# Performance work log

Hardware: AMD Instinct MI355X
Metric: run time of the kernel (lower is better)

## Reference

```python
import jax, jax.numpy as jnp
import numpy as np

NQ = 14            # n_qubits
NB = 2             # n_blocks
KLOC = 4           # k_local
K = 2 ** KLOC      # Hermitian observable dim = 16
NOFF = K * (K - 1) // 2   # 120 off-diagonal params
DEPTH = 3          # vqc_depth
IN_DIM = 784
OUT_DIM = 10
BATCH = 128
GROUPS = [list(range(s, s + KLOC)) for s in range(NQ - KLOC + 1)]  # sliding k-local groups
NOBS = len(GROUPS)  # 11
TOTAL_ENC = NB * ((NQ // 2) + ((NQ - 1) // 2)) * 15  # 390 SU(4) encoding params

# 15 two-qubit Pauli words in PennyLane's lexicographic IXYZ order (identity excluded)
_I = np.eye(2, dtype=np.complex64)
_X = np.array([[0, 1], [1, 0]], np.complex64)
_Y = np.array([[0, -1j], [1j, 0]], np.complex64)
_Z = np.array([[1, 0], [0, -1]], np.complex64)
_P = {'I': _I, 'X': _X, 'Y': _Y, 'Z': _Z}
_WORDS = [a + b for a in 'IXYZ' for b in 'IXYZ'][1:]
P15 = jnp.asarray(np.stack([np.kron(_P[w[0]], _P[w[1]]) for w in _WORDS]))  # (15,4,4)
CNOT = jnp.asarray(np.array([[1, 0, 0, 0], [0, 1, 0, 0], [0, 0, 0, 1], [0, 0, 1, 0]], np.complex64))
_ROWS, _COLS = np.tril_indices(K, -1)  # row-major lower-tri order == create_Hermitian fill order


def su4(theta):
    """PennyLane SpecialUnitary: U = expm(i * sum_m theta_m P_m), theta: (B,15).
    The generator is Hermitian, so use eigh instead of generic expm."""
    Hm = jnp.einsum('bm,mij->bij', theta.astype(jnp.complex64), P15)  # (B,4,4) Hermitian
    w, V = jnp.linalg.eigh(Hm)
    return jnp.einsum('bij,bj,bkj->bik', V, jnp.exp(1j * w.astype(jnp.complex64)), V.conj())


def apply_gate(state, U, wires):
    """Apply a k-qubit gate U ((B,2^k,2^k) or (2^k,2^k)) to state (B, 2,...,2)."""
    n = state.ndim - 1
    k = len(wires)
    axes = [w + 1 for w in wires]
    perm = [0] + axes + [a for a in range(1, n + 1) if a not in axes]
    st = jnp.transpose(state, perm)
    shp = st.shape
    st = st.reshape(shp[0], 2 ** k, -1)
    if U.ndim == 3:
        st = jnp.einsum('bij,bjr->bir', U, st)
    else:
        st = jnp.einsum('ij,bjr->bir', U, st)
    return jnp.transpose(st.reshape(shp), np.argsort(perm))


def expval_herm(state, H, wires):
    """<psi| H_{wires} |psi> per batch element."""
    n = state.ndim - 1
    axes = [w + 1 for w in wires]
    perm = [0] + axes + [a for a in range(1, n + 1) if a not in axes]
    st = jnp.transpose(state, perm).reshape(state.shape[0], H.shape[0], -1)
    return jnp.einsum('bkr,kl,blr->b', st.conj(), H, st).real


def create_hermitian(A, Bp, D):
    """Faithful port of create_Hermitian: lower-tri A+iB (row-major), diag D[1:] on
    positions 0..K-2 (D[0] unused, last diag 0), then H = h + h^dagger (diag doubled)."""
    h = jnp.zeros((K, K), jnp.complex64).at[_ROWS, _COLS].set(A + 1j * Bp)
    d = jnp.zeros((K,), A.dtype).at[jnp.arange(K - 1)].set(D[1:])
    h = h + jnp.diag(d).astype(jnp.complex64)
    return h + h.conj().T


def ry_mat(theta):
    c = jnp.cos(theta / 2)
    s = jnp.sin(theta / 2)
    return jnp.stack([jnp.stack([c, -s]), jnp.stack([s, c])]).astype(jnp.complex64)


def setup_inputs():
    key = jax.random.key(0)
    ks = jax.random.split(key, 9)
    lim = 1.0 / np.sqrt(IN_DIM)
    lim_h = 1.0 / np.sqrt(NOBS)
    return {
        'x': jax.random.normal(ks[0], (BATCH, IN_DIM), jnp.float32),
        'W_enc': jax.random.uniform(ks[1], (TOTAL_ENC, IN_DIM), jnp.float32, -lim, lim),
        'b_enc': jax.random.uniform(ks[2], (TOTAL_ENC,), jnp.float32, -lim, lim),
        'var_params': 0.01 * jax.random.normal(ks[3], (DEPTH, NQ), jnp.float32),
        'A': 2.0 * jax.random.normal(ks[4], (NOBS, NOFF), jnp.float32),
        'Bp': 2.0 * jax.random.normal(ks[5], (NOBS, NOFF), jnp.float32),
        'D': 2.0 * jax.random.normal(ks[6], (NOBS, K), jnp.float32),
        'W_head': jax.random.uniform(ks[7], (OUT_DIM, NOBS), jnp.float32, -lim_h, lim_h),
        'b_head': jax.random.uniform(ks[8], (OUT_DIM,), jnp.float32, -lim_h, lim_h),
    }


def reference(x, W_enc, b_enc, var_params, A, Bp, D, W_head, b_head):
    encoded = x @ W_enc.T + b_enc                      # (B, 390)
    Hs = jax.vmap(create_hermitian)(A, Bp, D)          # (NOBS, K, K)
    Bsz = x.shape[0]
    state = jnp.zeros((Bsz,) + (2,) * NQ, jnp.complex64).at[(slice(None),) + (0,) * NQ].set(1.0)
    # SU(4) brick-layer encoding: even pairs then odd pairs per block
    idx = 0
    for _ in range(NB):
        for q in list(range(0, NQ - 1, 2)) + list(range(1, NQ - 1, 2)):
            state = apply_gate(state, su4(encoded[:, idx:idx + 15]), [q, q + 1])
            idx += 15
    # variational RY + CNOT brick layers
    for layer in range(DEPTH):
        for q in range(NQ):
            state = apply_gate(state, ry_mat(var_params[layer, q]), [q])
        for q in list(range(0, NQ - 1, 2)) + list(range(1, NQ - 1, 2)):
            state = apply_gate(state, CNOT, [q, q + 1])
    q_out = jnp.stack([expval_herm(state, Hs[w], GROUPS[w]) for w in range(NOBS)], axis=1)
    q_out = q_out.astype(jnp.float32)                  # (B, NOBS)
    return q_out @ W_head.T + b_head                   # (B, OUT_DIM)
```

## Files before the change

kernel.cpp:

```cpp
#include <hip/hip_runtime.h>
#include <math.h>

#define NQ      14
#define NSTATE  16384
#define BATCH   128
#define DEPTH   3
#define NOBS    11
#define KDIM    16
#define NOFF    120
#define INDIM   784
#define OUTDIM  10

__device__ __forceinline__ int F2(int a) { return a + (a >> 4); }
#define PHYS2 (NSTATE + (NSTATE >> 4))

__device__ __forceinline__ float sbc(float x) {
  return __int_as_float(__builtin_amdgcn_readfirstlane(__float_as_int(x)));
}

__global__ __launch_bounds__(256) void enc_expm_kernel(
    const float* __restrict__ x, const float* __restrict__ W,
    const float* __restrict__ bvec, float2* __restrict__ Ubuf)
{
  int wave = ((blockIdx.x << 2) | (threadIdx.x >> 6));
  int lane = threadIdx.x & 63;
  int g = wave >> 7;
  int b = wave & 127;

  const float4* x4 = (const float4*)(x + (size_t)b * INDIM);
  const float4* w4 = (const float4*)(W + (size_t)g * 15 * INDIM);

  float acc[15];
#pragma unroll
  for (int m = 0; m < 15; ++m) acc[m] = 0.f;
#pragma unroll
  for (int it = 0; it < 4; ++it) {
    int j4 = lane + it * 64;
    if (j4 < 196) {
      float4 xv = x4[j4];
#pragma unroll
      for (int m = 0; m < 15; ++m) {
        float4 wv = w4[m * 196 + j4];
        acc[m] = fmaf(xv.x, wv.x, fmaf(xv.y, wv.y, fmaf(xv.z, wv.z, fmaf(xv.w, wv.w, acc[m]))));
      }
    }
  }
#pragma unroll
  for (int m = 0; m < 15; ++m) {
#pragma unroll
    for (int off = 32; off; off >>= 1) acc[m] += __shfl_xor(acc[m], off);
  }

  if (lane < 4) {
    const int j = lane;
    float th[15];
#pragma unroll
    for (int m = 0; m < 15; ++m) th[m] = acc[m] + bvec[g * 15 + m];

    const float pr_[4][4] = {{1,0,0,1},{0,1,1,0},{0,0,0,0},{1,0,0,-1}};
    const float pi_[4][4] = {{0,0,0,0},{0,0,0,0},{0,-1,1,0},{0,0,0,0}};
    float Hre[16], Him[16];
#pragma unroll
    for (int e = 0; e < 16; ++e) { Hre[e] = 0.f; Him[e] = 0.f; }
    float tsum = 0.f;
#pragma unroll
    for (int m = 0; m < 15; ++m) {
      float tv = th[m];
      tsum += fabsf(tv);
      const int code = m + 1;
      const int a = code >> 2, c = code & 3;
#pragma unroll
      for (int i = 0; i < 4; ++i)
#pragma unroll
        for (int jj = 0; jj < 4; ++jj) {
          float ar = pr_[a][(i >> 1) * 2 + (jj >> 1)], ai = pi_[a][(i >> 1) * 2 + (jj >> 1)];
          float br = pr_[c][(i & 1) * 2 + (jj & 1)],   bi = pi_[c][(i & 1) * 2 + (jj & 1)];
          Hre[i * 4 + jj] += tv * (ar * br - ai * bi);
          Him[i * 4 + jj] += tv * (ar * bi + ai * br);
        }
    }
    int s = 0;
    if (tsum > 0.25f) {
      s = (int)ceilf(log2f(tsum * 4.0f));
      if (s < 0) s = 0;
      if (s > 14) s = 14;
    }
    float sc = exp2f((float)(-s));
    float Gre[16], Gim[16];
#pragma unroll
    for (int e = 0; e < 16; ++e) { Gre[e] = -Him[e] * sc; Gim[e] = Hre[e] * sc; }

    float Tcr[4], Tci[4];
#pragma unroll
    for (int i = 0; i < 4; ++i) {
      Tcr[i] = Gre[i * 4 + j] * (1.f / 9.f) + ((i == j) ? 1.f : 0.f);
      Tci[i] = Gim[i * 4 + j] * (1.f / 9.f);
    }
#pragma unroll
    for (int k = 8; k >= 1; --k) {
      float nr[4], ni[4];
      float invk = 1.0f / (float)k;
#pragma unroll
      for (int i = 0; i < 4; ++i) {
        float xr = 0.f, xi = 0.f;
#pragma unroll
        for (int l = 0; l < 4; ++l) {
          xr = fmaf(Gre[i * 4 + l], Tcr[l], fmaf(-Gim[i * 4 + l], Tci[l], xr));
          xi = fmaf(Gre[i * 4 + l], Tci[l], fmaf( Gim[i * 4 + l], Tcr[l], xi));
        }
        nr[i] = invk * xr + ((i == j) ? 1.f : 0.f);
        ni[i] = invk * xi;
      }
#pragma unroll
      for (int i = 0; i < 4; ++i) { Tcr[i] = nr[i]; Tci[i] = ni[i]; }
    }
    for (int it = 0; it < s; ++it) {
      float nr[4] = {0.f, 0.f, 0.f, 0.f}, ni[4] = {0.f, 0.f, 0.f, 0.f};
#pragma unroll
      for (int l = 0; l < 4; ++l) {
        float tlr = Tcr[l], tli = Tci[l];
#pragma unroll
        for (int i = 0; i < 4; ++i) {
          float br = __shfl(Tcr[i], l);
          float bi = __shfl(Tci[i], l);
          nr[i] = fmaf(br, tlr, fmaf(-bi, tli, nr[i]));
          ni[i] = fmaf(br, tli, fmaf( bi, tlr, ni[i]));
        }
      }
#pragma unroll
      for (int i = 0; i < 4; ++i) { Tcr[i] = nr[i]; Tci[i] = ni[i]; }
    }
#pragma unroll
    for (int i = 0; i < 4; ++i)
      Ubuf[(size_t)wave * 16 + i * 4 + j] = make_float2(Tcr[i], Tci[i]);
  }
}

template<int S>
__device__ __forceinline__ int grpbase(int t) {
  return ((t >> S) << (S + 4)) | (t & ((1 << S) - 1));
}
template<int S>
__device__ __forceinline__ void ldgrp(const float2* st, int base, float* vr, float* vi) {
#pragma unroll
  for (int k = 0; k < 16; ++k) {
    float2 v = st[F2(base + (k << S))];
    vr[k] = v.x; vi[k] = v.y;
  }
}
template<int S>
__device__ __forceinline__ void stgrp(float2* st, int base, const float* vr, const float* vi) {
#pragma unroll
  for (int k = 0; k < 16; ++k) st[F2(base + (k << S))] = make_float2(vr[k], vi[k]);
}
__device__ __forceinline__ int base2s(int t) {
  return ((t >> 7) << 11) | (((t >> 5) & 3) << 7) | (t & 31);
}
__device__ __forceinline__ int addr2s(int base, int k) {
  return base + ((k >> 2) << 9) + ((k & 3) << 5);
}
__device__ __forceinline__ void ldgrp2(const float2* st, int base, float* vr, float* vi) {
#pragma unroll
  for (int k = 0; k < 16; ++k) {
    float2 v = st[F2(addr2s(base, k))];
    vr[k] = v.x; vi[k] = v.y;
  }
}
__device__ __forceinline__ void stgrp2(float2* st, int base, const float* vr, const float* vi) {
#pragma unroll
  for (int k = 0; k < 16; ++k) st[F2(addr2s(base, k))] = make_float2(vr[k], vi[k]);
}

__device__ __forceinline__ void loadU(const float2* __restrict__ Ug, float* ur, float* ui) {
#pragma unroll
  for (int e = 0; e < 16; ++e) {
    float2 u = Ug[e];
    ur[e] = sbc(u.x); ui[e] = sbc(u.y);
  }
}

__device__ __forceinline__ void applyU_hi(float* vr, float* vi, const float* ur, const float* ui) {
#pragma unroll
  for (int j2 = 0; j2 < 4; ++j2) {
    float ar[4], ai[4];
#pragma unroll
    for (int j = 0; j < 4; ++j) { ar[j] = vr[4 * j + j2]; ai[j] = vi[4 * j + j2]; }
#pragma unroll
    for (int i = 0; i < 4; ++i) {
      float xr = 0.f, xi = 0.f;
#pragma unroll
      for (int j = 0; j < 4; ++j) {
        xr = fmaf(ur[4 * i + j], ar[j], fmaf(-ui[4 * i + j], ai[j], xr));
        xi = fmaf(ur[4 * i + j], ai[j], fmaf( ui[4 * i + j], ar[j], xi));
      }
      vr[4 * i + j2] = xr; vi[4 * i + j2] = xi;
    }
  }
}
__device__ __forceinline__ void applyU_lo(float* vr, float* vi, const float* ur, const float* ui) {
#pragma unroll
  for (int i2 = 0; i2 < 4; ++i2) {
    float ar[4], ai[4];
#pragma unroll
    for (int j = 0; j < 4; ++j) { ar[j] = vr[4 * i2 + j]; ai[j] = vi[4 * i2 + j]; }
#pragma unroll
    for (int i = 0; i < 4; ++i) {
      float xr = 0.f, xi = 0.f;
#pragma unroll
      for (int j = 0; j < 4; ++j) {
        xr = fmaf(ur[4 * i + j], ar[j], fmaf(-ui[4 * i + j], ai[j], xr));
        xi = fmaf(ur[4 * i + j], ai[j], fmaf( ui[4 * i + j], ar[j], xi));
      }
      vr[4 * i2 + i] = xr; vi[4 * i2 + i] = xi;
    }
  }
}
__device__ __forceinline__ void applyU_mid(float* vr, float* vi, const float* ur, const float* ui) {
#pragma unroll
  for (int o = 0; o < 4; ++o) {
    const int kb = ((o >> 1) << 3) | (o & 1);
    float ar[4], ai[4];
#pragma unroll
    for (int j = 0; j < 4; ++j) { ar[j] = vr[kb | (j << 1)]; ai[j] = vi[kb | (j << 1)]; }
#pragma unroll
    for (int i = 0; i < 4; ++i) {
      float xr = 0.f, xi = 0.f;
#pragma unroll
      for (int j = 0; j < 4; ++j) {
        xr = fmaf(ur[4 * i + j], ar[j], fmaf(-ui[4 * i + j], ai[j], xr));
        xi = fmaf(ur[4 * i + j], ai[j], fmaf( ui[4 * i + j], ar[j], xi));
      }
      vr[kb | (i << 1)] = xr; vi[kb | (i << 1)] = xi;
    }
  }
}

template<int B>
__device__ __forceinline__ void ry16(float* vr, float* vi, float c, float s) {
#pragma unroll
  for (int k = 0; k < 16; ++k) {
    if (!(k & (1 << B))) {
      const int k1 = k | (1 << B);
      float r0 = vr[k], i0 = vi[k], r1 = vr[k1], i1 = vi[k1];
      vr[k]  = fmaf(c, r0, -s * r1);  vi[k]  = fmaf(c, i0, -s * i1);
      vr[k1] = fmaf(s, r0,  c * r1);  vi[k1] = fmaf(s, i0,  c * i1);
    }
  }
}
template<int CB, int TB>
__device__ __forceinline__ void cx16(float* vr, float* vi) {
#pragma unroll
  for (int k = 0; k < 16; ++k) {
    if ((k & (1 << CB)) && !(k & (1 << TB))) {
      const int k1 = k | (1 << TB);
      float tr = vr[k]; vr[k] = vr[k1]; vr[k1] = tr;
      float ti = vi[k]; vi[k] = vi[k1]; vi[k1] = ti;
    }
  }
}

template<int S>
__device__ __forceinline__ void enc_pass3(float2* st, const float2* __restrict__ U,
                                          int gHi, int gLo, int gMid, int b, int t) {
  float ur[16], ui[16], vr[16], vi[16];
  int base = grpbase<S>(t);
  ldgrp<S>(st, base, vr, vi);
  loadU(U + ((size_t)gHi  * BATCH + b) * 16, ur, ui); applyU_hi (vr, vi, ur, ui);
  loadU(U + ((size_t)gLo  * BATCH + b) * 16, ur, ui); applyU_lo (vr, vi, ur, ui);
  loadU(U + ((size_t)gMid * BATCH + b) * 16, ur, ui); applyU_mid(vr, vi, ur, ui);
  stgrp<S>(st, base, vr, vi);
}
__device__ __forceinline__ void enc_passD(float2* st, const float2* __restrict__ U,
                                          int gLo, int gMid, int b, int t) {
  float ur[16], ui[16], vr[16], vi[16];
  int base = t << 4;
  ldgrp<0>(st, base, vr, vi);
  loadU(U + ((size_t)gLo  * BATCH + b) * 16, ur, ui); applyU_lo (vr, vi, ur, ui);
  loadU(U + ((size_t)gMid * BATCH + b) * 16, ur, ui); applyU_mid(vr, vi, ur, ui);
  stgrp<0>(st, base, vr, vi);
}
__device__ __forceinline__ void enc_passE(float2* st, const float2* __restrict__ U,
                                          int gA, int gB, int b, int t) {
  float ur[16], ui[16], vr[16], vi[16];
  int base = base2s(t);
  ldgrp2(st, base, vr, vi);
  loadU(U + ((size_t)gA * BATCH + b) * 16, ur, ui); applyU_hi(vr, vi, ur, ui);
  loadU(U + ((size_t)gB * BATCH + b) * 16, ur, ui); applyU_lo(vr, vi, ur, ui);
  stgrp2(st, base, vr, vi);
}
template<int S>
__device__ __forceinline__ void var_pass3(float2* st, const float* __restrict__ vp,
                                          int l, int qbase, int t) {
  float vr[16], vi[16];
  int base = grpbase<S>(t);
  ldgrp<S>(st, base, vr, vi);
  float c[4], sn[4];
#pragma unroll
  for (int i = 0; i < 4; ++i) {
    float a = sbc(vp[l * NQ + qbase + i]) * 0.5f;
    c[i] = cosf(a); sn[i] = sinf(a);
  }
  ry16<3>(vr, vi, c[0], sn[0]);
  ry16<2>(vr, vi, c[1], sn[1]);
  ry16<1>(vr, vi, c[2], sn[2]);
  ry16<0>(vr, vi, c[3], sn[3]);
  cx16<3, 2>(vr, vi);
  cx16<1, 0>(vr, vi);
  cx16<2, 1>(vr, vi);
  stgrp<S>(st, base, vr, vi);
}
__device__ __forceinline__ void var_passD(float2* st, const float* __restrict__ vp,
                                          int l, int t) {
  float vr[16], vi[16];
  int base = t << 4;
  ldgrp<0>(st, base, vr, vi);
  float a0 = sbc(vp[l * NQ + 12]) * 0.5f;
  float a1 = sbc(vp[l * NQ + 13]) * 0.5f;
  ry16<1>(vr, vi, cosf(a0), sinf(a0));
  ry16<0>(vr, vi, cosf(a1), sinf(a1));
  cx16<1, 0>(vr, vi);
  cx16<2, 1>(vr, vi);
  stgrp<0>(st, base, vr, vi);
}
__device__ __forceinline__ void var_passE(float2* st, int t) {
  float vr[16], vi[16];
  int base = base2s(t);
  ldgrp2(st, base, vr, vi);
  cx16<3, 2>(vr, vi);
  cx16<1, 0>(vr, vi);
  stgrp2(st, base, vr, vi);
}

__global__ __launch_bounds__(1024) void qsim_kernel(
    const float2* __restrict__ U, const float* __restrict__ var_params,
    const float* __restrict__ A, const float* __restrict__ Bp,
    const float* __restrict__ D, const float* __restrict__ Wh,
    const float* __restrict__ bh, float* __restrict__ out)
{
  __shared__ float2 st[PHYS2];
  __shared__ float red[6][16];

  const int t = threadIdx.x;
  const int b = blockIdx.x >> 1;
  const int h = blockIdx.x & 1;
  const int nw = h ? 5 : 6;

  for (int i = t; i < PHYS2; i += 1024)
    st[i] = (i == 0) ? make_float2(1.f, 0.f) : make_float2(0.f, 0.f);
  __syncthreads();

  for (int nb = 0; nb < 2; ++nb) {
    int gI = nb * 13;
    enc_pass3<10>(st, U, gI + 0, gI + 1, gI + 7,  b, t); __syncthreads();
    enc_pass3<6 >(st, U, gI + 2, gI + 3, gI + 9,  b, t); __syncthreads();
    enc_pass3<2 >(st, U, gI + 4, gI + 5, gI + 11, b, t); __syncthreads();
    enc_passD    (st, U, gI + 6, gI + 12,         b, t); __syncthreads();
    enc_passE    (st, U, gI + 8, gI + 10,         b, t); __syncthreads();
  }

  for (int l = 0; l < DEPTH; ++l) {
    var_pass3<10>(st, var_params, l, 0, t); __syncthreads();
    var_pass3<6 >(st, var_params, l, 4, t); __syncthreads();
    var_pass3<2 >(st, var_params, l, 8, t); __syncthreads();
    var_passD    (st, var_params, l,    t); __syncthreads();
    var_passE    (st, t);                   __syncthreads();
  }

  const int wave = t >> 6;
  for (int idx = 0; idx < nw; ++idx) {
    const int w = 2 * idx + h;
    const float* __restrict__ Aw = A + w * NOFF;
    const float* __restrict__ Bw = Bp + w * NOFF;
    const float* __restrict__ Dw = D + w * KDIM;
    const int shift = 10 - w;
    const int hi2 = t >> shift;
    const int lo = t & ((1 << shift) - 1);
    const int base2 = (hi2 << (shift + 4)) | lo;
    float sr[16], si[16];
#pragma unroll
    for (int k = 0; k < 16; ++k) {
      float2 v = st[F2(base2 + (k << shift))];
      sr[k] = v.x; si[k] = v.y;
    }
    float yr[16], yi[16];
#pragma unroll
    for (int k = 0; k < 16; ++k) {
      float dk = (k < 15) ? Dw[k + 1] : 0.f;
      yr[k] = dk * sr[k];
      yi[k] = dk * si[k];
    }
#pragma unroll
    for (int k = 1; k < 16; ++k) {
#pragma unroll
      for (int l2 = 0; l2 < k; ++l2) {
        const int pidx = (k * (k - 1)) / 2 + l2;
        const float a = Aw[pidx];
        const float q = Bw[pidx];
        yr[k] = fmaf(a, sr[l2], fmaf(-q, si[l2], yr[k]));
        yi[k] = fmaf(a, si[l2], fmaf( q, sr[l2], yi[k]));
      }
    }
    float E = 0.f;
#pragma unroll
    for (int k = 0; k < 16; ++k)
      E = fmaf(sr[k], yr[k], fmaf(si[k], yi[k], E));
    E *= 2.0f;
#pragma unroll
    for (int off = 32; off; off >>= 1) E += __shfl_xor(E, off);
    if ((t & 63) == 0) red[idx][wave] = E;
  }
  __syncthreads();

  if (t < OUTDIM) {
    float o = (h == 0) ? bh[t] : 0.f;
    for (int idx = 0; idx < nw; ++idx) {
      const int w = 2 * idx + h;
      float q = 0.f;
#pragma unroll
      for (int ww = 0; ww < 16; ++ww) q += red[idx][ww];
      o = fmaf(Wh[t * NOBS + w], q, o);
    }
    atomicAdd(&out[b * OUTDIM + t], o);
  }
}

extern "C" void kernel_launch(void* const* d_in, const int* in_sizes, int n_in,
                              void* d_out, int out_size, void* d_ws, size_t ws_size,
                              hipStream_t stream) {
  const float* x          = (const float*)d_in[0];
  const float* W_enc      = (const float*)d_in[1];
  const float* b_enc      = (const float*)d_in[2];
  const float* var_params = (const float*)d_in[3];
  const float* A          = (const float*)d_in[4];
  const float* Bp         = (const float*)d_in[5];
  const float* D          = (const float*)d_in[6];
  const float* W_head     = (const float*)d_in[7];
  const float* b_head     = (const float*)d_in[8];
  float* out = (float*)d_out;

  float2* Ubuf = (float2*)d_ws;

  hipMemsetAsync(out, 0, (size_t)out_size * sizeof(float), stream);
  enc_expm_kernel<<<832, 256, 0, stream>>>(x, W_enc, b_enc, Ubuf);
  qsim_kernel<<<256, 1024, 0, stream>>>(Ubuf, var_params, A, Bp, D,
                                        W_head, b_head, out);
}
```

Baseline: 188.0 us.

## Split encoding GEMV and SU(4) expm into separate kernels with dense lanes

```diff
diff --git a/kernel.cpp b/kernel.cpp
--- a/kernel.cpp
+++ b/kernel.cpp
@@ -18,9 +18,9 @@
   return __int_as_float(__builtin_amdgcn_readfirstlane(__float_as_int(x)));
 }
 
-__global__ __launch_bounds__(256) void enc_expm_kernel(
+__global__ __launch_bounds__(256) void enc_kernel(
     const float* __restrict__ x, const float* __restrict__ W,
-    const float* __restrict__ bvec, float2* __restrict__ Ubuf)
+    const float* __restrict__ bvec, float* __restrict__ theta)
 {
   int wave = ((blockIdx.x << 2) | (threadIdx.x >> 6));
   int lane = threadIdx.x & 63;
@@ -50,90 +50,101 @@
 #pragma unroll
     for (int off = 32; off; off >>= 1) acc[m] += __shfl_xor(acc[m], off);
   }
-
-  if (lane < 4) {
-    const int j = lane;
-    float th[15];
-#pragma unroll
-    for (int m = 0; m < 15; ++m) th[m] = acc[m] + bvec[g * 15 + m];
-
-    const float pr_[4][4] = {{1,0,0,1},{0,1,1,0},{0,0,0,0},{1,0,0,-1}};
-    const float pi_[4][4] = {{0,0,0,0},{0,0,0,0},{0,-1,1,0},{0,0,0,0}};
-    float Hre[16], Him[16];
-#pragma unroll
-    for (int e = 0; e < 16; ++e) { Hre[e] = 0.f; Him[e] = 0.f; }
-    float tsum = 0.f;
-#pragma unroll
-    for (int m = 0; m < 15; ++m) {
-      float tv = th[m];
-      tsum += fabsf(tv);
-      const int code = m + 1;
-      const int a = code >> 2, c = code & 3;
-#pragma unroll
-      for (int i = 0; i < 4; ++i)
-#pragma unroll
-        for (int jj = 0; jj < 4; ++jj) {
-          float ar = pr_[a][(i >> 1) * 2 + (jj >> 1)], ai = pi_[a][(i >> 1) * 2 + (jj >> 1)];
-          float br = pr_[c][(i & 1) * 2 + (jj & 1)],   bi = pi_[c][(i & 1) * 2 + (jj & 1)];
-          Hre[i * 4 + jj] += tv * (ar * br - ai * bi);
-          Him[i * 4 + jj] += tv * (ar * bi + ai * br);
-        }
-    }
-    int s = 0;
-    if (tsum > 0.25f) {
-      s = (int)ceilf(log2f(tsum * 4.0f));
-      if (s < 0) s = 0;
-      if (s > 14) s = 14;
-    }
-    float sc = exp2f((float)(-s));
-    float Gre[16], Gim[16];
-#pragma unroll
-    for (int e = 0; e < 16; ++e) { Gre[e] = -Him[e] * sc; Gim[e] = Hre[e] * sc; }
-
-    float Tcr[4], Tci[4];
+  if (lane == 0) {
+#pragma unroll
+    for (int m = 0; m < 15; ++m) theta[(size_t)wave * 15 + m] = acc[m] + bvec[g * 15 + m];
+  }
+}
+
+__global__ __launch_bounds__(256) void expm_kernel(
+    const float* __restrict__ theta, float2* __restrict__ Ubuf)
+{
+  int gid  = blockIdx.x * 256 + threadIdx.x;
+  int pair = gid >> 2;
+  int j    = gid & 3;
+  int lane = threadIdx.x & 63;
+  int grp  = lane & 60;
+
+  const float* th = theta + (size_t)pair * 15;
+
+  const float pr_[4][4] = {{1,0,0,1},{0,1,1,0},{0,0,0,0},{1,0,0,-1}};
+  const float pi_[4][4] = {{0,0,0,0},{0,0,0,0},{0,-1,1,0},{0,0,0,0}};
+
+  float Hre[16], Him[16];
+#pragma unroll
+  for (int e = 0; e < 16; ++e) { Hre[e] = 0.f; Him[e] = 0.f; }
+  float tsum = 0.f;
+#pragma unroll
+  for (int m = 0; m < 15; ++m) {
+    float tv = th[m];
+    tsum += fabsf(tv);
+    const int code = m + 1;
+    const int a = code >> 2, c = code & 3;
+#pragma unroll
+    for (int i = 0; i < 4; ++i)
+#pragma unroll
+      for (int jj = 0; jj < 4; ++jj) {
+        float ar = pr_[a][(i >> 1) * 2 + (jj >> 1)], ai = pi_[a][(i >> 1) * 2 + (jj >> 1)];
+        float br = pr_[c][(i & 1) * 2 + (jj & 1)],   bi = pi_[c][(i & 1) * 2 + (jj & 1)];
+        Hre[i * 4 + jj] += tv * (ar * br - ai * bi);
+        Him[i * 4 + jj] += tv * (ar * bi + ai * br);
+      }
+  }
+  int s = 0;
+  if (tsum > 0.25f) {
+    s = (int)ceilf(log2f(tsum * 4.0f));
+    if (s < 0) s = 0;
+    if (s > 14) s = 14;
+  }
+  float sc = exp2f((float)(-s));
+  float Gre[16], Gim[16];
+#pragma unroll
+  for (int e = 0; e < 16; ++e) { Gre[e] = -Him[e] * sc; Gim[e] = Hre[e] * sc; }
+
+  float Tcr[4], Tci[4];
+#pragma unroll
+  for (int i = 0; i < 4; ++i) {
+    Tcr[i] = Gre[i * 4 + j] * (1.f / 9.f) + ((i == j) ? 1.f : 0.f);
+    Tci[i] = Gim[i * 4 + j] * (1.f / 9.f);
+  }
+#pragma unroll
+  for (int k = 8; k >= 1; --k) {
+    float nr[4], ni[4];
+    float invk = 1.0f / (float)k;
 #pragma unroll
     for (int i = 0; i < 4; ++i) {
-      Tcr[i] = Gre[i * 4 + j] * (1.f / 9.f) + ((i == j) ? 1.f : 0.f);
-      Tci[i] = Gim[i * 4 + j] * (1.f / 9.f);
-    }
-#pragma unroll
-    for (int k = 8; k >= 1; --k) {
-      float nr[4], ni[4];
-      float invk = 1.0f / (float)k;
+      float xr = 0.f, xi = 0.f;
+#pragma unroll
+      for (int l = 0; l < 4; ++l) {
+        xr = fmaf(Gre[i * 4 + l], Tcr[l], fmaf(-Gim[i * 4 + l], Tci[l], xr));
+        xi = fmaf(Gre[i * 4 + l], Tci[l], fmaf( Gim[i * 4 + l], Tcr[l], xi));
+      }
+      nr[i] = invk * xr + ((i == j) ? 1.f : 0.f);
+      ni[i] = invk * xi;
+    }
+#pragma unroll
+    for (int i = 0; i < 4; ++i) { Tcr[i] = nr[i]; Tci[i] = ni[i]; }
+  }
+  for (int it = 0; it < s; ++it) {
+    float nr[4] = {0.f, 0.f, 0.f, 0.f}, ni[4] = {0.f, 0.f, 0.f, 0.f};
+#pragma unroll
+    for (int l = 0; l < 4; ++l) {
+      int src = grp | l;
+      float tlr = Tcr[l], tli = Tci[l];
 #pragma unroll
       for (int i = 0; i < 4; ++i) {
-        float xr = 0.f, xi = 0.f;
-#pragma unroll
-        for (int l = 0; l < 4; ++l) {
-          xr = fmaf(Gre[i * 4 + l], Tcr[l], fmaf(-Gim[i * 4 + l], Tci[l], xr));
-          xi = fmaf(Gre[i * 4 + l], Tci[l], fmaf( Gim[i * 4 + l], Tcr[l], xi));
-        }
-        nr[i] = invk * xr + ((i == j) ? 1.f : 0.f);
-        ni[i] = invk * xi;
-      }
-#pragma unroll
-      for (int i = 0; i < 4; ++i) { Tcr[i] = nr[i]; Tci[i] = ni[i]; }
-    }
-    for (int it = 0; it < s; ++it) {
-      float nr[4] = {0.f, 0.f, 0.f, 0.f}, ni[4] = {0.f, 0.f, 0.f, 0.f};
-#pragma unroll
-      for (int l = 0; l < 4; ++l) {
-        float tlr = Tcr[l], tli = Tci[l];
-#pragma unroll
-        for (int i = 0; i < 4; ++i) {
-          float br = __shfl(Tcr[i], l);
-          float bi = __shfl(Tci[i], l);
-          nr[i] = fmaf(br, tlr, fmaf(-bi, tli, nr[i]));
-          ni[i] = fmaf(br, tli, fmaf( bi, tlr, ni[i]));
-        }
-      }
-#pragma unroll
-      for (int i = 0; i < 4; ++i) { Tcr[i] = nr[i]; Tci[i] = ni[i]; }
-    }
-#pragma unroll
-    for (int i = 0; i < 4; ++i)
-      Ubuf[(size_t)wave * 16 + i * 4 + j] = make_float2(Tcr[i], Tci[i]);
-  }
+        float br = __shfl(Tcr[i], src);
+        float bi = __shfl(Tci[i], src);
+        nr[i] = fmaf(br, tlr, fmaf(-bi, tli, nr[i]));
+        ni[i] = fmaf(br, tli, fmaf( bi, tlr, ni[i]));
+      }
+    }
+#pragma unroll
+    for (int i = 0; i < 4; ++i) { Tcr[i] = nr[i]; Tci[i] = ni[i]; }
+  }
+#pragma unroll
+  for (int i = 0; i < 4; ++i)
+    Ubuf[(size_t)pair * 16 + i * 4 + j] = make_float2(Tcr[i], Tci[i]);
 }
 
 template<int S>
@@ -438,10 +449,13 @@
   const float* b_head     = (const float*)d_in[8];
   float* out = (float*)d_out;
 
-  float2* Ubuf = (float2*)d_ws;
+  float*  theta = (float*)d_ws;
+  size_t  thBytes = (size_t)3328 * 15 * sizeof(float);
+  float2* Ubuf = (float2*)((char*)d_ws + ((thBytes + 255) / 256) * 256);
 
   hipMemsetAsync(out, 0, (size_t)out_size * sizeof(float), stream);
-  enc_expm_kernel<<<832, 256, 0, stream>>>(x, W_enc, b_enc, Ubuf);
+  enc_kernel <<<832, 256, 0, stream>>>(x, W_enc, b_enc, theta);
+  expm_kernel<<<52,  256, 0, stream>>>(theta, Ubuf);
   qsim_kernel<<<256, 1024, 0, stream>>>(Ubuf, var_params, A, Bp, D,
                                         W_head, b_head, out);
 }
```

Measured after the change: 176.6 us. 6.1% less time.

## Fuse SU(4) encoding expm into simulation kernel and add separate head kernel

Applied to the files above, without the earlier changes.

```diff
diff --git a/kernel.cpp b/kernel.cpp
--- a/kernel.cpp
+++ b/kernel.cpp
@@ -18,124 +18,6 @@
   return __int_as_float(__builtin_amdgcn_readfirstlane(__float_as_int(x)));
 }
 
-__global__ __launch_bounds__(256) void enc_expm_kernel(
-    const float* __restrict__ x, const float* __restrict__ W,
-    const float* __restrict__ bvec, float2* __restrict__ Ubuf)
-{
-  int wave = ((blockIdx.x << 2) | (threadIdx.x >> 6));
-  int lane = threadIdx.x & 63;
-  int g = wave >> 7;
-  int b = wave & 127;
-
-  const float4* x4 = (const float4*)(x + (size_t)b * INDIM);
-  const float4* w4 = (const float4*)(W + (size_t)g * 15 * INDIM);
-
-  float acc[15];
-#pragma unroll
-  for (int m = 0; m < 15; ++m) acc[m] = 0.f;
-#pragma unroll
-  for (int it = 0; it < 4; ++it) {
-    int j4 = lane + it * 64;
-    if (j4 < 196) {
-      float4 xv = x4[j4];
-#pragma unroll
-      for (int m = 0; m < 15; ++m) {
-        float4 wv = w4[m * 196 + j4];
-        acc[m] = fmaf(xv.x, wv.x, fmaf(xv.y, wv.y, fmaf(xv.z, wv.z, fmaf(xv.w, wv.w, acc[m]))));
-      }
-    }
-  }
-#pragma unroll
-  for (int m = 0; m < 15; ++m) {
-#pragma unroll
-    for (int off = 32; off; off >>= 1) acc[m] += __shfl_xor(acc[m], off);
-  }
-
-  if (lane < 4) {
-    const int j = lane;
-    float th[15];
-#pragma unroll
-    for (int m = 0; m < 15; ++m) th[m] = acc[m] + bvec[g * 15 + m];
-
-    const float pr_[4][4] = {{1,0,0,1},{0,1,1,0},{0,0,0,0},{1,0,0,-1}};
-    const float pi_[4][4] = {{0,0,0,0},{0,0,0,0},{0,-1,1,0},{0,0,0,0}};
-    float Hre[16], Him[16];
-#pragma unroll
-    for (int e = 0; e < 16; ++e) { Hre[e] = 0.f; Him[e] = 0.f; }
-    float tsum = 0.f;
-#pragma unroll
-    for (int m = 0; m < 15; ++m) {
-      float tv = th[m];
-      tsum += fabsf(tv);
-      const int code = m + 1;
-      const int a = code >> 2, c = code & 3;
-#pragma unroll
-      for (int i = 0; i < 4; ++i)
-#pragma unroll
-        for (int jj = 0; jj < 4; ++jj) {
-          float ar = pr_[a][(i >> 1) * 2 + (jj >> 1)], ai = pi_[a][(i >> 1) * 2 + (jj >> 1)];
-          float br = pr_[c][(i & 1) * 2 + (jj & 1)],   bi = pi_[c][(i & 1) * 2 + (jj & 1)];
-          Hre[i * 4 + jj] += tv * (ar * br - ai * bi);
-          Him[i * 4 + jj] += tv * (ar * bi + ai * br);
-        }
-    }
-    int s = 0;
-    if (tsum > 0.25f) {
-      s = (int)ceilf(log2f(tsum * 4.0f));
-      if (s < 0) s = 0;
-      if (s > 14) s = 14;
-    }
-    float sc = exp2f((float)(-s));
-    float Gre[16], Gim[16];
-#pragma unroll
-    for (int e = 0; e < 16; ++e) { Gre[e] = -Him[e] * sc; Gim[e] = Hre[e] * sc; }
-
-    float Tcr[4], Tci[4];
-#pragma unroll
-    for (int i = 0; i < 4; ++i) {
-      Tcr[i] = Gre[i * 4 + j] * (1.f / 9.f) + ((i == j) ? 1.f : 0.f);
-      Tci[i] = Gim[i * 4 + j] * (1.f / 9.f);
-    }
-#pragma unroll
-    for (int k = 8; k >= 1; --k) {
-      float nr[4], ni[4];
-      float invk = 1.0f / (float)k;
-#pragma unroll
-      for (int i = 0; i < 4; ++i) {
-        float xr = 0.f, xi = 0.f;
-#pragma unroll
-        for (int l = 0; l < 4; ++l) {
-          xr = fmaf(Gre[i * 4 + l], Tcr[l], fmaf(-Gim[i * 4 + l], Tci[l], xr));
-          xi = fmaf(Gre[i * 4 + l], Tci[l], fmaf( Gim[i * 4 + l], Tcr[l], xi));
-        }
-        nr[i] = invk * xr + ((i == j) ? 1.f : 0.f);
-        ni[i] = invk * xi;
-      }
-#pragma unroll
-      for (int i = 0; i < 4; ++i) { Tcr[i] = nr[i]; Tci[i] = ni[i]; }
-    }
-    for (int it = 0; it < s; ++it) {
-      float nr[4] = {0.f, 0.f, 0.f, 0.f}, ni[4] = {0.f, 0.f, 0.f, 0.f};
-#pragma unroll
-      for (int l = 0; l < 4; ++l) {
-        float tlr = Tcr[l], tli = Tci[l];
-#pragma unroll
-        for (int i = 0; i < 4; ++i) {
-          float br = __shfl(Tcr[i], l);
-          float bi = __shfl(Tci[i], l);
-          nr[i] = fmaf(br, tlr, fmaf(-bi, tli, nr[i]));
-          ni[i] = fmaf(br, tli, fmaf( bi, tlr, ni[i]));
-        }
-      }
-#pragma unroll
-      for (int i = 0; i < 4; ++i) { Tcr[i] = nr[i]; Tci[i] = ni[i]; }
-    }
-#pragma unroll
-    for (int i = 0; i < 4; ++i)
-      Ubuf[(size_t)wave * 16 + i * 4 + j] = make_float2(Tcr[i], Tci[i]);
-  }
-}
-
 template<int S>
 __device__ __forceinline__ int grpbase(int t) {
   return ((t >> S) << (S + 4)) | (t & ((1 << S) - 1));
@@ -171,11 +53,11 @@
   for (int k = 0; k < 16; ++k) st[F2(addr2s(base, k))] = make_float2(vr[k], vi[k]);
 }
 
-__device__ __forceinline__ void loadU(const float2* __restrict__ Ug, float* ur, float* ui) {
+__device__ __forceinline__ void loadU(const float2* Ul, float* ur, float* ui) {
 #pragma unroll
   for (int e = 0; e < 16; ++e) {
-    float2 u = Ug[e];
-    ur[e] = sbc(u.x); ui[e] = sbc(u.y);
+    float2 u = Ul[e];
+    ur[e] = u.x; ui[e] = u.y;
   }
 }
 
@@ -260,32 +142,32 @@
 }
 
 template<int S>
-__device__ __forceinline__ void enc_pass3(float2* st, const float2* __restrict__ U,
-                                          int gHi, int gLo, int gMid, int b, int t) {
+__device__ __forceinline__ void enc_pass3(float2* st, const float2* Ulds,
+                                          int gHi, int gLo, int gMid, int t) {
   float ur[16], ui[16], vr[16], vi[16];
   int base = grpbase<S>(t);
   ldgrp<S>(st, base, vr, vi);
-  loadU(U + ((size_t)gHi  * BATCH + b) * 16, ur, ui); applyU_hi (vr, vi, ur, ui);
-  loadU(U + ((size_t)gLo  * BATCH + b) * 16, ur, ui); applyU_lo (vr, vi, ur, ui);
-  loadU(U + ((size_t)gMid * BATCH + b) * 16, ur, ui); applyU_mid(vr, vi, ur, ui);
+  loadU(Ulds + gHi  * 16, ur, ui); applyU_hi (vr, vi, ur, ui);
+  loadU(Ulds + gLo  * 16, ur, ui); applyU_lo (vr, vi, ur, ui);
+  loadU(Ulds + gMid * 16, ur, ui); applyU_mid(vr, vi, ur, ui);
   stgrp<S>(st, base, vr, vi);
 }
-__device__ __forceinline__ void enc_passD(float2* st, const float2* __restrict__ U,
-                                          int gLo, int gMid, int b, int t) {
+__device__ __forceinline__ void enc_passD(float2* st, const float2* Ulds,
+                                          int gLo, int gMid, int t) {
   float ur[16], ui[16], vr[16], vi[16];
   int base = t << 4;
   ldgrp<0>(st, base, vr, vi);
-  loadU(U + ((size_t)gLo  * BATCH + b) * 16, ur, ui); applyU_lo (vr, vi, ur, ui);
-  loadU(U + ((size_t)gMid * BATCH + b) * 16, ur, ui); applyU_mid(vr, vi, ur, ui);
+  loadU(Ulds + gLo  * 16, ur, ui); applyU_lo (vr, vi, ur, ui);
+  loadU(Ulds + gMid * 16, ur, ui); applyU_mid(vr, vi, ur, ui);
   stgrp<0>(st, base, vr, vi);
 }
-__device__ __forceinline__ void enc_passE(float2* st, const float2* __restrict__ U,
-                                          int gA, int gB, int b, int t) {
+__device__ __forceinline__ void enc_passE(float2* st, const float2* Ulds,
+                                          int gA, int gB, int t) {
   float ur[16], ui[16], vr[16], vi[16];
   int base = base2s(t);
   ldgrp2(st, base, vr, vi);
-  loadU(U + ((size_t)gA * BATCH + b) * 16, ur, ui); applyU_hi(vr, vi, ur, ui);
-  loadU(U + ((size_t)gB * BATCH + b) * 16, ur, ui); applyU_lo(vr, vi, ur, ui);
+  loadU(Ulds + gA * 16, ur, ui); applyU_hi(vr, vi, ur, ui);
+  loadU(Ulds + gB * 16, ur, ui); applyU_lo(vr, vi, ur, ui);
   stgrp2(st, base, vr, vi);
 }
 template<int S>
@@ -331,31 +213,146 @@
   stgrp2(st, base, vr, vi);
 }
 
-__global__ __launch_bounds__(1024) void qsim_kernel(
-    const float2* __restrict__ U, const float* __restrict__ var_params,
+__global__ __launch_bounds__(1024) void qfm_kernel(
+    const float* __restrict__ x, const float* __restrict__ W,
+    const float* __restrict__ bvec, const float* __restrict__ var_params,
     const float* __restrict__ A, const float* __restrict__ Bp,
-    const float* __restrict__ D, const float* __restrict__ Wh,
-    const float* __restrict__ bh, float* __restrict__ out)
+    const float* __restrict__ D, float* __restrict__ qws)
 {
   __shared__ float2 st[PHYS2];
+  __shared__ float2 Ulds[26 * 16];
   __shared__ float red[6][16];
 
   const int t = threadIdx.x;
   const int b = blockIdx.x >> 1;
   const int h = blockIdx.x & 1;
   const int nw = h ? 5 : 6;
+  const int wv = t >> 6;
+  const int lane = t & 63;
 
   for (int i = t; i < PHYS2; i += 1024)
     st[i] = (i == 0) ? make_float2(1.f, 0.f) : make_float2(0.f, 0.f);
+
+  const float4* x4 = (const float4*)(x + (size_t)b * INDIM);
+  for (int r = 0; r < 2; ++r) {
+    const int g = r * 13 + wv;
+    if (wv < 13) {
+      const float4* w4 = (const float4*)(W + (size_t)g * 15 * INDIM);
+      float acc[15];
+#pragma unroll
+      for (int m = 0; m < 15; ++m) acc[m] = 0.f;
+#pragma unroll
+      for (int it = 0; it < 4; ++it) {
+        int j4 = lane + it * 64;
+        if (j4 < 196) {
+          float4 xv = x4[j4];
+#pragma unroll
+          for (int m = 0; m < 15; ++m) {
+            float4 wvv = w4[m * 196 + j4];
+            acc[m] = fmaf(xv.x, wvv.x, fmaf(xv.y, wvv.y, fmaf(xv.z, wvv.z, fmaf(xv.w, wvv.w, acc[m]))));
+          }
+        }
+      }
+#pragma unroll
+      for (int m = 0; m < 15; ++m) {
+#pragma unroll
+        for (int off = 32; off; off >>= 1) acc[m] += __shfl_xor(acc[m], off);
+      }
+
+      if (lane < 4) {
+        const int j = lane;
+        float th[15];
+#pragma unroll
+        for (int m = 0; m < 15; ++m) th[m] = acc[m] + bvec[g * 15 + m];
+
+        const float pr_[4][4] = {{1,0,0,1},{0,1,1,0},{0,0,0,0},{1,0,0,-1}};
+        const float pi_[4][4] = {{0,0,0,0},{0,0,0,0},{0,-1,1,0},{0,0,0,0}};
+        float Hre[16], Him[16];
+#pragma unroll
+        for (int e = 0; e < 16; ++e) { Hre[e] = 0.f; Him[e] = 0.f; }
+        float tsum = 0.f;
+#pragma unroll
+        for (int m = 0; m < 15; ++m) {
+          float tv = th[m];
+          tsum += fabsf(tv);
+          const int code = m + 1;
+          const int a = code >> 2, c = code & 3;
+#pragma unroll
+          for (int i = 0; i < 4; ++i)
+#pragma unroll
+            for (int jj = 0; jj < 4; ++jj) {
+              float ar = pr_[a][(i >> 1) * 2 + (jj >> 1)], ai = pi_[a][(i >> 1) * 2 + (jj >> 1)];
+              float br = pr_[c][(i & 1) * 2 + (jj & 1)],   bi = pi_[c][(i & 1) * 2 + (jj & 1)];
+              Hre[i * 4 + jj] += tv * (ar * br - ai * bi);
+              Him[i * 4 + jj] += tv * (ar * bi + ai * br);
+            }
+        }
+        int s = 0;
+        if (tsum > 0.25f) {
+          s = (int)ceilf(log2f(tsum * 4.0f));
+          if (s < 0) s = 0;
+          if (s > 14) s = 14;
+        }
+        float sc = exp2f((float)(-s));
+        float Gre[16], Gim[16];
+#pragma unroll
+        for (int e = 0; e < 16; ++e) { Gre[e] = -Him[e] * sc; Gim[e] = Hre[e] * sc; }
+
+        float Tcr[4], Tci[4];
+#pragma unroll
+        for (int i = 0; i < 4; ++i) {
+          Tcr[i] = Gre[i * 4 + j] * (1.f / 9.f) + ((i == j) ? 1.f : 0.f);
+          Tci[i] = Gim[i * 4 + j] * (1.f / 9.f);
+        }
+#pragma unroll
+        for (int k = 8; k >= 1; --k) {
+          float nr[4], ni[4];
+          float invk = 1.0f / (float)k;
+#pragma unroll
+          for (int i = 0; i < 4; ++i) {
+            float xr = 0.f, xi = 0.f;
+#pragma unroll
+            for (int l = 0; l < 4; ++l) {
+              xr = fmaf(Gre[i * 4 + l], Tcr[l], fmaf(-Gim[i * 4 + l], Tci[l], xr));
+              xi = fmaf(Gre[i * 4 + l], Tci[l], fmaf( Gim[i * 4 + l], Tcr[l], xi));
+            }
+            nr[i] = invk * xr + ((i == j) ? 1.f : 0.f);
+            ni[i] = invk * xi;
+          }
+#pragma unroll
+          for (int i = 0; i < 4; ++i) { Tcr[i] = nr[i]; Tci[i] = ni[i]; }
+        }
+        for (int it = 0; it < s; ++it) {
+          float nr[4] = {0.f, 0.f, 0.f, 0.f}, ni[4] = {0.f, 0.f, 0.f, 0.f};
+#pragma unroll
+          for (int l = 0; l < 4; ++l) {
+            float tlr = Tcr[l], tli = Tci[l];
+#pragma unroll
+            for (int i = 0; i < 4; ++i) {
+              float br = __shfl(Tcr[i], l);
+              float bi = __shfl(Tci[i], l);
+              nr[i] = fmaf(br, tlr, fmaf(-bi, tli, nr[i]));
+              ni[i] = fmaf(br, tli, fmaf( bi, tlr, ni[i]));
+            }
+          }
+#pragma unroll
+          for (int i = 0; i < 4; ++i) { Tcr[i] = nr[i]; Tci[i] = ni[i]; }
+        }
+#pragma unroll
+        for (int i = 0; i < 4; ++i)
+          Ulds[g * 16 + i * 4 + j] = make_float2(Tcr[i], Tci[i]);
+      }
+    }
+  }
   __syncthreads();
 
   for (int nb = 0; nb < 2; ++nb) {
     int gI = nb * 13;
-    enc_pass3<10>(st, U, gI + 0, gI + 1, gI + 7,  b, t); __syncthreads();
-    enc_pass3<6 >(st, U, gI + 2, gI + 3, gI + 9,  b, t); __syncthreads();
-    enc_pass3<2 >(st, U, gI + 4, gI + 5, gI + 11, b, t); __syncthreads();
-    enc_passD    (st, U, gI + 6, gI + 12,         b, t); __syncthreads();
-    enc_passE    (st, U, gI + 8, gI + 10,         b, t); __syncthreads();
+    enc_pass3<10>(st, Ulds, gI + 0, gI + 1, gI + 7,  t); __syncthreads();
+    enc_pass3<6 >(st, Ulds, gI + 2, gI + 3, gI + 9,  t); __syncthreads();
+    enc_pass3<2 >(st, Ulds, gI + 4, gI + 5, gI + 11, t); __syncthreads();
+    enc_passD    (st, Ulds, gI + 6, gI + 12,         t); __syncthreads();
+    enc_passE    (st, Ulds, gI + 8, gI + 10,         t); __syncthreads();
   }
 
   for (int l = 0; l < DEPTH; ++l) {
@@ -366,7 +363,6 @@
     var_passE    (st, t);                   __syncthreads();
   }
 
-  const int wave = t >> 6;
   for (int idx = 0; idx < nw; ++idx) {
     const int w = 2 * idx + h;
     const float* __restrict__ Aw = A + w * NOFF;
@@ -407,21 +403,31 @@
     E *= 2.0f;
 #pragma unroll
     for (int off = 32; off; off >>= 1) E += __shfl_xor(E, off);
-    if ((t & 63) == 0) red[idx][wave] = E;
+    if ((t & 63) == 0) red[idx][wv] = E;
   }
   __syncthreads();
 
-  if (t < OUTDIM) {
-    float o = (h == 0) ? bh[t] : 0.f;
-    for (int idx = 0; idx < nw; ++idx) {
-      const int w = 2 * idx + h;
-      float q = 0.f;
-#pragma unroll
-      for (int ww = 0; ww < 16; ++ww) q += red[idx][ww];
-      o = fmaf(Wh[t * NOBS + w], q, o);
-    }
-    atomicAdd(&out[b * OUTDIM + t], o);
-  }
+  if (t < nw) {
+    float q = 0.f;
+#pragma unroll
+    for (int ww = 0; ww < 16; ++ww) q += red[t][ww];
+    qws[b * 16 + 2 * t + h] = q;
+  }
+}
+
+__global__ __launch_bounds__(256) void head_kernel(
+    const float* __restrict__ qws, const float* __restrict__ Wh,
+    const float* __restrict__ bh, float* __restrict__ out)
+{
+  int idx = blockIdx.x * 256 + threadIdx.x;
+  if (idx >= BATCH * OUTDIM) return;
+  int b = idx / OUTDIM;
+  int o = idx - b * OUTDIM;
+  float v = bh[o];
+#pragma unroll
+  for (int w = 0; w < NOBS; ++w)
+    v = fmaf(Wh[o * NOBS + w], qws[b * 16 + w], v);
+  out[idx] = v;
 }
 
 extern "C" void kernel_launch(void* const* d_in, const int* in_sizes, int n_in,
@@ -438,10 +444,9 @@
   const float* b_head     = (const float*)d_in[8];
   float* out = (float*)d_out;
 
-  float2* Ubuf = (float2*)d_ws;
-
-  hipMemsetAsync(out, 0, (size_t)out_size * sizeof(float), stream);
-  enc_expm_kernel<<<832, 256, 0, stream>>>(x, W_enc, b_enc, Ubuf);
-  qsim_kernel<<<256, 1024, 0, stream>>>(Ubuf, var_params, A, Bp, D,
-                                        W_head, b_head, out);
-}
+  float* qws = (float*)d_ws;
+
+  qfm_kernel <<<256, 1024, 0, stream>>>(x, W_enc, b_enc, var_params,
+                                        A, Bp, D, qws);
+  head_kernel<<<5, 256, 0, stream>>>(qws, W_head, b_head, out);
+}
```

Result: slower. 201.4 us (+7.2%).
